# Kernel optimization log

Hardware: AMD Instinct MI355X
Metric: run time of the kernel (lower is better)

Reference implementation:

```python
import jax, jax.numpy as jnp
from jax import lax
import numpy as np

B, N, K = 8, 4096, 64          # clouds, points per cloud, max neighbors
N1, N2 = N // 2, N // 8        # fps ratio 0.5, then 0.25
R1, R2 = 0.2, 0.4              # ball-query radii


def setup_inputs() -> dict:
    key = jax.random.key(0)
    ks = jax.random.split(key, 7)
    def w(k, i, o):
        return jax.random.normal(k, (i, o), jnp.float32) / np.sqrt(i).astype(np.float32)
    return {
        "pos": jax.random.uniform(ks[0], (B, N, 3), jnp.float32),
        "w1a": w(ks[1], 3, 64),    "b1a": jnp.zeros(64, jnp.float32),
        "w1b": w(ks[2], 64, 64),   "b1b": jnp.zeros(64, jnp.float32),
        "w2a": w(ks[3], 67, 128),  "b2a": jnp.zeros(128, jnp.float32),
        "w2b": w(ks[4], 128, 128), "b2b": jnp.zeros(128, jnp.float32),
        "w3a": w(ks[5], 131, 256), "b3a": jnp.zeros(256, jnp.float32),
        "w3b": w(ks[6], 256, 1024),"b3b": jnp.zeros(1024, jnp.float32),
    }


def fps(pos, n_samples):
    # farthest point sampling, deterministic start at index 0. pos: [n, 3]
    d0 = jnp.sum((pos - pos[0]) ** 2, axis=-1)
    def step(mind, _):
        nxt = jnp.argmax(mind)
        d = jnp.sum((pos - pos[nxt]) ** 2, axis=-1)
        return jnp.minimum(mind, d), nxt
    _, idxs = lax.scan(step, d0, None, length=n_samples - 1)
    return jnp.concatenate([jnp.zeros((1,), idxs.dtype), idxs])


def ball_query(centers, pts, r):
    # up to K neighbors within radius r (nearest-first); centers are a subset of pts
    d2 = jnp.sum((centers[:, None, :] - pts[None, :, :]) ** 2, axis=-1)  # [M, n]
    neg = jnp.where(d2 <= r * r, -d2, -jnp.inf)
    vals, nbr = lax.top_k(neg, K)
    return nbr, vals > -jnp.inf  # [M, K] indices, validity mask


def mlp(x, w1, b1, w2, b2, relu_last):
    h = jax.nn.relu(x @ w1 + b1) @ w2 + b2
    return jax.nn.relu(h) if relu_last else h


def masked_max(h, mask):
    # max over neighbor axis; every center has itself as a valid neighbor
    return jnp.max(jnp.where(mask[..., None], h, -jnp.inf), axis=1)


def reference(pos, w1a, b1a, w1b, b1b, w2a, b2a, w2b, b2b, w3a, b3a, w3b, b3b):
    def single(p):  # p: [N, 3]
        # SA1: x is None -> per-edge input is relative position only
        idx1 = fps(p, N1)
        c1 = p[idx1]                                   # [N1, 3]
        nbr1, m1 = ball_query(c1, p, R1)               # [N1, K]
        rel1 = p[nbr1] - c1[:, None, :]                # [N1, K, 3]
        x1 = masked_max(mlp(rel1, w1a, b1a, w1b, b1b, True), m1)   # [N1, 64]
        # SA2: per-edge input is [x_j, pos_j - pos_i]
        idx2 = fps(c1, N2)
        c2 = c1[idx2]                                  # [N2, 3]
        nbr2, m2 = ball_query(c2, c1, R2)              # [N2, K]
        feat2 = jnp.concatenate([x1[nbr2], c1[nbr2] - c2[:, None, :]], axis=-1)  # [N2,K,67]
        x2 = masked_max(mlp(feat2, w2a, b2a, w2b, b2b, True), m2)  # [N2, 128]
        # Global SA: MLP on [x, pos] then global max pool
        g = mlp(jnp.concatenate([x2, c2], axis=-1), w3a, b3a, w3b, b3b, False)   # [N2,1024]
        return jnp.max(g, axis=0)                      # [1024]
    return jax.vmap(single)(pos)                       # [B, 1024]
```

## Files before the change

### kernel.cpp

```cpp
#include <hip/hip_runtime.h>
#include <cstdint>
#include <cstddef>


static constexpr int Bc = 8;
static constexpr int Np = 4096;
static constexpr int Kn = 64;
static constexpr int M1 = 2048;
static constexpr int M2 = 512;
static constexpr int LDX = 132;

#define DEVINL __device__ __forceinline__

DEVINL float d2_exact(float ax, float ay, float az, float bx, float by, float bz) {
    float dx = __fsub_rn(ax, bx);
    float dy = __fsub_rn(ay, by);
    float dz = __fsub_rn(az, bz);
    float xx = __fmul_rn(dx, dx);
    float yy = __fmul_rn(dy, dy);
    float zz = __fmul_rn(dz, dz);
    return __fadd_rn(__fadd_rn(xx, yy), zz);
}

template <int CTRL, int RM, int BM>
DEVINL unsigned long long dpp_max_step(unsigned long long k) {
    unsigned lo = (unsigned)k, hi = (unsigned)(k >> 32);
    unsigned slo = (unsigned)__builtin_amdgcn_update_dpp(0, (int)lo, CTRL, RM, BM, true);
    unsigned shi = (unsigned)__builtin_amdgcn_update_dpp(0, (int)hi, CTRL, RM, BM, true);
    unsigned long long s = ((unsigned long long)shi << 32) | (unsigned long long)slo;
    return s > k ? s : k;
}

DEVINL unsigned long long wave_max_u64_dpp(unsigned long long k) {
    k = dpp_max_step<0x111, 0xf, 0xf>(k);
    k = dpp_max_step<0x112, 0xf, 0xf>(k);
    k = dpp_max_step<0x114, 0xf, 0xf>(k);
    k = dpp_max_step<0x118, 0xf, 0xf>(k);
    k = dpp_max_step<0x142, 0xa, 0xf>(k);
    k = dpp_max_step<0x143, 0xc, 0xf>(k);
    return k;
}

DEVINL unsigned mort3(unsigned v) {
    return (v & 1u) | ((v & 2u) << 2) | ((v & 4u) << 4);
}

DEVINL unsigned cell_of(float x, float y, float z) {
    int ix = (int)(x * 8.0f); ix = ix < 0 ? 0 : (ix > 7 ? 7 : ix);
    int iy = (int)(y * 8.0f); iy = iy < 0 ? 0 : (iy > 7 ? 7 : iy);
    int iz = (int)(z * 8.0f); iz = iz < 0 ? 0 : (iz > 7 ? 7 : iz);
    return mort3((unsigned)ix) | (mort3((unsigned)iy) << 1) | (mort3((unsigned)iz) << 2);
}

DEVINL unsigned* scan512(unsigned* h0, unsigned* h1, int t) {
    unsigned* src = h0; unsigned* dst = h1;
    for (int d = 1; d < 512; d <<= 1) {
        unsigned v = src[t];
        if (t >= d) v += src[t - d];
        dst[t] = v;
        __syncthreads();
        unsigned* tmp = src; src = dst; dst = tmp;
    }
    return src;
}

__global__ __launch_bounds__(512)
void fps2x_kernel(const float* __restrict__ pos, float* __restrict__ c1,
                  float* __restrict__ c2, float* __restrict__ X) {
    constexpr int NT = 512;
    __shared__ float scx[Np], scy[Np], scz[Np];
    __shared__ unsigned spk[Np];
    __shared__ float s2c[M1 * 3];
    __shared__ unsigned h0[512], h1[512];
    __shared__ unsigned long long slots[3];
    const int b = blockIdx.x;
    const int t = threadIdx.x;
    const int lane = t & 63;

    {
        constexpr int PT = Np / NT;
        const float* base = pos + (size_t)b * Np * 3;
        float gx[PT], gy[PT], gz[PT];
        unsigned gc[PT];
        #pragma unroll
        for (int j = 0; j < PT; ++j) {
            int p = j * NT + t;
            gx[j] = base[p * 3 + 0];
            gy[j] = base[p * 3 + 1];
            gz[j] = base[p * 3 + 2];
            gc[j] = cell_of(gx[j], gy[j], gz[j]);
        }
        float x0 = base[0], y0 = base[1], z0 = base[2];
        h0[t] = 0;
        if (t == 0) { slots[0] = 0; slots[1] = 0; slots[2] = 0; }
        __syncthreads();
        #pragma unroll
        for (int j = 0; j < PT; ++j) atomicAdd(&h0[gc[j]], 1u);
        __syncthreads();
        unsigned cnt = h0[t];
        unsigned* inc = scan512(h0, h1, t);
        inc[t] -= cnt;
        __syncthreads();
        #pragma unroll
        for (int j = 0; j < PT; ++j) {
            unsigned p = atomicAdd(&inc[gc[j]], 1u);
            scx[p] = gx[j]; scy[p] = gy[j]; scz[p] = gz[j];
            spk[p] = ((0xFFFu - (unsigned)(j * NT + t)) << 12) | p;
        }
        __syncthreads();

        float px[PT], py[PT], pz[PT], mind[PT];
        unsigned oi[PT];
        #pragma unroll
        for (int j = 0; j < PT; ++j) {
            int p = t * PT + j;
            px[j] = scx[p]; py[j] = scy[p]; pz[j] = scz[p];
            oi[j] = spk[p];
        }
        float lox = px[0], hix = px[0], loy = py[0], hiy = py[0], loz = pz[0], hiz = pz[0];
        #pragma unroll
        for (int j = 1; j < PT; ++j) {
            lox = fminf(lox, px[j]); hix = fmaxf(hix, px[j]);
            loy = fminf(loy, py[j]); hiy = fmaxf(hiy, py[j]);
            loz = fminf(loz, pz[j]); hiz = fmaxf(hiz, pz[j]);
        }

        unsigned long long ck = 0;
        #pragma unroll
        for (int j = 0; j < PT; ++j) {
            float d = d2_exact(px[j], py[j], pz[j], x0, y0, z0);
            mind[j] = d;
            unsigned long long kj =
                ((unsigned long long)__float_as_uint(d) << 24) | (unsigned long long)oi[j];
            if (kj > ck) ck = kj;
        }
        float bmax = __uint_as_float((unsigned)(ck >> 24));
        unsigned long long wkey = wave_max_u64_dpp(ck);
        if (lane == 63) atomicMax(&slots[1], wkey);
        if (t == 0) {
            s2c[0] = x0; s2c[1] = y0; s2c[2] = z0;
        }
        int rd = 1, wr = 2, rs = 0;
        for (int s = 1; s < M1; ++s) {
            __syncthreads();
            unsigned long long km = slots[rd];
            if (t == 0) slots[rs] = 0;
            unsigned spos = (unsigned)km & 0xFFFu;
            float cx = scx[spos], cy = scy[spos], cz = scz[spos];
            if (t == 0) {
                s2c[s * 3 + 0] = cx; s2c[s * 3 + 1] = cy; s2c[s * 3 + 2] = cz;
            }
            float dxv = fmaxf(fmaxf(lox - cx, cx - hix), 0.0f);
            float dyv = fmaxf(fmaxf(loy - cy, cy - hiy), 0.0f);
            float dzv = fmaxf(fmaxf(loz - cz, cz - hiz), 0.0f);
            float L = dxv * dxv + dyv * dyv + dzv * dzv;
            bool fire = (L * 0.999f <= bmax);
            if (fire) {
                unsigned long long nck = 0;
                #pragma unroll
                for (int j = 0; j < PT; ++j) {
                    float d = d2_exact(px[j], py[j], pz[j], cx, cy, cz);
                    float m = fminf(mind[j], d);
                    mind[j] = m;
                    unsigned long long kj =
                        ((unsigned long long)__float_as_uint(m) << 24) | (unsigned long long)oi[j];
                    if (kj > nck) nck = kj;
                }
                ck = nck;
                bmax = __uint_as_float((unsigned)(ck >> 24));
            }
            if (__ballot(fire) != 0ull) wkey = wave_max_u64_dpp(ck);
            if (lane == 63) atomicMax(&slots[wr], wkey);
            int nrd = wr; wr = rs; rs = rd; rd = nrd;
        }
    }
    __syncthreads();

    for (int i = t; i < M1 * 3; i += 512)
        c1[(size_t)b * M1 * 3 + i] = s2c[i];

    {
        constexpr int PT = M1 / NT;
        float* c2buf = s2c;
        float gx[PT], gy[PT], gz[PT];
        unsigned gc[PT];
        #pragma unroll
        for (int j = 0; j < PT; ++j) {
            int p = j * NT + t;
            gx[j] = s2c[p * 3 + 0];
            gy[j] = s2c[p * 3 + 1];
            gz[j] = s2c[p * 3 + 2];
            gc[j] = cell_of(gx[j], gy[j], gz[j]);
        }
        float x0 = s2c[0], y0 = s2c[1], z0 = s2c[2];
        h0[t] = 0;
        if (t == 0) { slots[0] = 0; slots[1] = 0; slots[2] = 0; }
        __syncthreads();
        #pragma unroll
        for (int j = 0; j < PT; ++j) atomicAdd(&h0[gc[j]], 1u);
        __syncthreads();
        unsigned cnt = h0[t];
        unsigned* inc = scan512(h0, h1, t);
        inc[t] -= cnt;
        __syncthreads();
        #pragma unroll
        for (int j = 0; j < PT; ++j) {
            unsigned p = atomicAdd(&inc[gc[j]], 1u);
            scx[p] = gx[j]; scy[p] = gy[j]; scz[p] = gz[j];
            spk[p] = ((0xFFFu - (unsigned)(j * NT + t)) << 12) | p;
        }
        __syncthreads();

        float px[PT], py[PT], pz[PT], mind[PT];
        unsigned oi[PT];
        #pragma unroll
        for (int j = 0; j < PT; ++j) {
            int p = t * PT + j;
            px[j] = scx[p]; py[j] = scy[p]; pz[j] = scz[p];
            oi[j] = spk[p];
        }
        float lox = px[0], hix = px[0], loy = py[0], hiy = py[0], loz = pz[0], hiz = pz[0];
        #pragma unroll
        for (int j = 1; j < PT; ++j) {
            lox = fminf(lox, px[j]); hix = fmaxf(hix, px[j]);
            loy = fminf(loy, py[j]); hiy = fmaxf(hiy, py[j]);
            loz = fminf(loz, pz[j]); hiz = fmaxf(hiz, pz[j]);
        }

        unsigned long long ck = 0;
        #pragma unroll
        for (int j = 0; j < PT; ++j) {
            float d = d2_exact(px[j], py[j], pz[j], x0, y0, z0);
            mind[j] = d;
            unsigned long long kj =
                ((unsigned long long)__float_as_uint(d) << 24) | (unsigned long long)oi[j];
            if (kj > ck) ck = kj;
        }
        float bmax = __uint_as_float((unsigned)(ck >> 24));
        unsigned long long wkey = wave_max_u64_dpp(ck);
        if (lane == 63) atomicMax(&slots[1], wkey);
        if (t == 0) {
            c2buf[0] = x0; c2buf[1] = y0; c2buf[2] = z0;
        }
        int rd = 1, wr = 2, rs = 0;
        for (int s = 1; s < M2; ++s) {
            __syncthreads();
            unsigned long long km = slots[rd];
            if (t == 0) slots[rs] = 0;
            unsigned spos = (unsigned)km & 0xFFFu;
            float cx = scx[spos], cy = scy[spos], cz = scz[spos];
            if (t == 0) {
                c2buf[s * 3 + 0] = cx; c2buf[s * 3 + 1] = cy; c2buf[s * 3 + 2] = cz;
            }
            float dxv = fmaxf(fmaxf(lox - cx, cx - hix), 0.0f);
            float dyv = fmaxf(fmaxf(loy - cy, cy - hiy), 0.0f);
            float dzv = fmaxf(fmaxf(loz - cz, cz - hiz), 0.0f);
            float L = dxv * dxv + dyv * dyv + dzv * dzv;
            bool fire = (L * 0.999f <= bmax);
            if (fire) {
                unsigned long long nck = 0;
                #pragma unroll
                for (int j = 0; j < PT; ++j) {
                    float d = d2_exact(px[j], py[j], pz[j], cx, cy, cz);
                    float m = fminf(mind[j], d);
                    mind[j] = m;
                    unsigned long long kj =
                        ((unsigned long long)__float_as_uint(m) << 24) | (unsigned long long)oi[j];
                    if (kj > nck) nck = kj;
                }
                ck = nck;
                bmax = __uint_as_float((unsigned)(ck >> 24));
            }
            if (__ballot(fire) != 0ull) wkey = wave_max_u64_dpp(ck);
            if (lane == 63) atomicMax(&slots[wr], wkey);
            int nrd = wr; wr = rs; rs = rd; rd = nrd;
        }
        __syncthreads();

        for (int i = t; i < M2 * 3; i += 512)
            c2[(size_t)b * M2 * 3 + i] = c2buf[i];
        for (int i = t; i < M2 * 3; i += 512) {
            int s = i / 3, k = i - s * 3;
            X[(size_t)(b * M2 + s) * LDX + 128 + k] = c2buf[i];
        }
    }
}

template <int NPT>
__global__ __launch_bounds__(256)
void bq_kernel(const float* __restrict__ pts, const float* __restrict__ ctr,
               int mshift, float r2, int* __restrict__ nbr) {
    constexpr int CH = NPT / 64;
    constexpr int CAP = 1024;
    __shared__ uint2 cbuf[4][CAP];
    const int lane = threadIdx.x & 63;
    const int wl = threadIdx.x >> 6;
    int w = __builtin_amdgcn_readfirstlane((int)(blockIdx.x * 4 + wl));
    const int b = w >> mshift;
    const float* pb = pts + (size_t)b * NPT * 3;
    const float* cp = ctr + (size_t)w * 3;
    float cx = cp[0], cy = cp[1], cz = cp[2];
    const unsigned r2b = __float_as_uint(r2);

    unsigned ub[CH];
    int cnt = 0;
    #pragma unroll
    for (int j = 0; j < CH; ++j) {
        int p = j * 64 + lane;
        float d = d2_exact(pb[p * 3 + 0], pb[p * 3 + 1], pb[p * 3 + 2], cx, cy, cz);
        ub[j] = __float_as_uint(d);
        cnt += __popcll(__ballot(ub[j] <= r2b));
    }
    int* out = nbr + (size_t)w * Kn;
    const unsigned long long lml = (1ull << lane) - 1ull;

    if (cnt <= Kn) {
        int basep = 0;
        #pragma unroll
        for (int j = 0; j < CH; ++j) {
            bool v = ub[j] <= r2b;
            unsigned long long mk = __ballot(v);
            if (v) out[basep + __popcll(mk & lml)] = j * 64 + lane;
            basep += __popcll(mk);
        }
        if (lane >= cnt) out[lane] = -1;
    } else if (cnt <= CAP) {
        uint2* buf = cbuf[wl];
        int basep = 0;
        #pragma unroll
        for (int j = 0; j < CH; ++j) {
            bool v = ub[j] <= r2b;
            unsigned long long mk = __ballot(v);
            if (v) buf[basep + __popcll(mk & lml)] =
                       make_uint2(ub[j], (unsigned)(j * 64 + lane));
            basep += __popcll(mk);
        }
        const int C2 = (cnt + 63) >> 6;
        unsigned cb[CAP / 64], ci[CAP / 64];
        #pragma unroll
        for (int e = 0; e < CAP / 64; ++e) {
            if (e >= C2) break;
            int p = e * 64 + lane;
            uint2 v = buf[p];
            cb[e] = (p < cnt) ? v.x : 0xFFFFFFFFu;
            ci[e] = v.y;
        }
        unsigned lo = 0, hi = r2b;
        while (lo < hi) {
            unsigned mid = lo + ((hi - lo) >> 1);
            int c = 0;
            #pragma unroll
            for (int e = 0; e < CAP / 64; ++e) {
                if (e >= C2) break;
                c += __popcll(__ballot(cb[e] <= mid));
            }
            if (c >= Kn) hi = mid; else lo = mid + 1;
        }
        const unsigned tt = lo;
        int cntLess = 0;
        #pragma unroll
        for (int e = 0; e < CAP / 64; ++e) {
            if (e >= C2) break;
            cntLess += __popcll(__ballot(cb[e] < tt));
        }
        const int quota = Kn - cntLess;
        int baseLt = 0, eqseen = 0;
        #pragma unroll
        for (int e = 0; e < CAP / 64; ++e) {
            if (e >= C2) break;
            bool lt = cb[e] < tt;
            bool eq = cb[e] == tt;
            unsigned long long mlt = __ballot(lt);
            unsigned long long meq = __ballot(eq);
            if (lt) out[baseLt + __popcll(mlt & lml)] = (int)ci[e];
            if (eq) {
                int rr = eqseen + __popcll(meq & lml);
                if (rr < quota) out[cntLess + rr] = (int)ci[e];
            }
            baseLt += __popcll(mlt);
            eqseen += __popcll(meq);
        }
    } else {
        unsigned lo = 0, hi = r2b;
        while (lo < hi) {
            unsigned mid = lo + ((hi - lo) >> 1);
            int c = 0;
            #pragma unroll
            for (int j = 0; j < CH; ++j) c += __popcll(__ballot(ub[j] <= mid));
            if (c >= Kn) hi = mid; else lo = mid + 1;
        }
        const unsigned tt = lo;
        int cntLess = 0;
        #pragma unroll
        for (int j = 0; j < CH; ++j) cntLess += __popcll(__ballot(ub[j] < tt));
        const int quota = Kn - cntLess;
        int baseLt = 0, eqseen = 0;
        #pragma unroll
        for (int j = 0; j < CH; ++j) {
            bool lt = ub[j] < tt;
            bool eq = ub[j] == tt;
            unsigned long long mlt = __ballot(lt);
            unsigned long long meq = __ballot(eq);
            if (lt) out[baseLt + __popcll(mlt & lml)] = j * 64 + lane;
            if (eq) {
                int rr = eqseen + __popcll(meq & lml);
                if (rr < quota) out[cntLess + rr] = j * 64 + lane;
            }
            baseLt += __popcll(mlt);
            eqseen += __popcll(meq);
        }
    }
}

__global__ __launch_bounds__(256)
void mlp1_kernel(const float* __restrict__ pos, const float* __restrict__ c1,
                 const int* __restrict__ nbr, const float* __restrict__ w1aT,
                 const float* __restrict__ w1bT, const float* __restrict__ b1b,
                 float* __restrict__ x1) {
    const int lane = threadIdx.x & 63;
    int w = __builtin_amdgcn_readfirstlane((int)(blockIdx.x * 4 + (threadIdx.x >> 6)));
    const int b = w >> 11;
    const int ii = nbr[(size_t)w * Kn + lane];
    const bool valid = ii >= 0;
    const int i2 = valid ? ii : 0;
    const float* pp = pos + ((size_t)b * Np + i2) * 3;
    const float* cc = c1 + (size_t)w * 3;
    float rx = pp[0] - cc[0], ry = pp[1] - cc[1], rz = pp[2] - cc[2];
    float h1[64];
    #pragma unroll
    for (int h = 0; h < 64; ++h) {
        float4 wv = ((const float4*)w1aT)[h];
        float a = fmaf(rx, wv.x, fmaf(ry, wv.y, fmaf(rz, wv.z, wv.w)));
        h1[h] = fmaxf(a, 0.0f);
    }
    float* orow = x1 + (size_t)w * 64;
    for (int c4 = 0; c4 < 16; ++c4) {
        float v4[4];
        #pragma unroll
        for (int cq = 0; cq < 4; ++cq) {
            int c = c4 * 4 + cq;
            float acc = b1b[c];
            const float4* wr = (const float4*)(w1bT + (size_t)c * 64);
            #pragma unroll
            for (int q = 0; q < 16; ++q) {
                float4 wv = wr[q];
                acc = fmaf(h1[4 * q + 0], wv.x, acc);
                acc = fmaf(h1[4 * q + 1], wv.y, acc);
                acc = fmaf(h1[4 * q + 2], wv.z, acc);
                acc = fmaf(h1[4 * q + 3], wv.w, acc);
            }
            float v = fmaxf(acc, 0.0f);
            v = valid ? v : -__builtin_inff();
            #pragma unroll
            for (int o = 32; o > 0; o >>= 1) v = fmaxf(v, __shfl_xor(v, o, 64));
            v4[cq] = v;
        }
        if (lane == 0)
            ((float4*)orow)[c4] = make_float4(v4[0], v4[1], v4[2], v4[3]);
    }
}

__global__ __launch_bounds__(256)
void mlp2_kernel(const float* __restrict__ x1, const float* __restrict__ c1,
                 const float* __restrict__ c2, const int* __restrict__ nbr2,
                 const float* __restrict__ w2aT, const float* __restrict__ w2bT,
                 const float* __restrict__ b2b, float* __restrict__ X) {
    const int lane = threadIdx.x & 63;
    int w = __builtin_amdgcn_readfirstlane((int)(blockIdx.x * 4 + (threadIdx.x >> 6)));
    const int b = w >> 9;
    const int ii = nbr2[(size_t)w * Kn + lane];
    const bool valid = ii >= 0;
    const int i2 = valid ? ii : 0;

    float x[68];
    const float4* xr = (const float4*)(x1 + ((size_t)b * M1 + i2) * 64);
    #pragma unroll
    for (int q = 0; q < 16; ++q) {
        float4 v = xr[q];
        x[4 * q + 0] = v.x; x[4 * q + 1] = v.y;
        x[4 * q + 2] = v.z; x[4 * q + 3] = v.w;
    }
    const float* cc = c2 + (size_t)w * 3;
    const float* cp = c1 + ((size_t)b * M1 + i2) * 3;
    x[64] = cp[0] - cc[0];
    x[65] = cp[1] - cc[1];
    x[66] = cp[2] - cc[2];
    x[67] = 0.0f;

    float h1[128];
    #pragma unroll
    for (int h = 0; h < 128; ++h) {
        const float4* r4 = (const float4*)(w2aT + (size_t)h * 80);
        float acc = 0.0f;
        #pragma unroll
        for (int q = 0; q < 16; ++q) {
            float4 wv = r4[q];
            acc = fmaf(x[4 * q + 0], wv.x, acc);
            acc = fmaf(x[4 * q + 1], wv.y, acc);
            acc = fmaf(x[4 * q + 2], wv.z, acc);
            acc = fmaf(x[4 * q + 3], wv.w, acc);
        }
        float4 tl = r4[16];
        acc = fmaf(x[64], tl.x, acc);
        acc = fmaf(x[65], tl.y, acc);
        acc = fmaf(x[66], tl.z, acc);
        acc += tl.w;
        h1[h] = fmaxf(acc, 0.0f);
    }
    float* orow = X + (size_t)w * LDX;
    for (int c4 = 0; c4 < 32; ++c4) {
        float v4[4];
        #pragma unroll
        for (int cq = 0; cq < 4; ++cq) {
            int c = c4 * 4 + cq;
            float acc = b2b[c];
            const float4* wr = (const float4*)(w2bT + (size_t)c * 128);
            #pragma unroll
            for (int q = 0; q < 32; ++q) {
                float4 wv = wr[q];
                acc = fmaf(h1[4 * q + 0], wv.x, acc);
                acc = fmaf(h1[4 * q + 1], wv.y, acc);
                acc = fmaf(h1[4 * q + 2], wv.z, acc);
                acc = fmaf(h1[4 * q + 3], wv.w, acc);
            }
            float v = fmaxf(acc, 0.0f);
            v = valid ? v : -__builtin_inff();
            #pragma unroll
            for (int o = 32; o > 0; o >>= 1) v = fmaxf(v, __shfl_xor(v, o, 64));
            v4[cq] = v;
        }
        if (lane == 0) {
            orow[c4 * 4 + 0] = v4[0]; orow[c4 * 4 + 1] = v4[1];
            orow[c4 * 4 + 2] = v4[2]; orow[c4 * 4 + 3] = v4[3];
        }
    }
}

__global__ __launch_bounds__(256)
void gemm1_kernel(const float* __restrict__ X, const float* __restrict__ w3a,
                  const float* __restrict__ b3a, float* __restrict__ H) {
    const int r = blockIdx.x;
    const int c = threadIdx.x;
    const float* xr = X + (size_t)r * LDX;
    float acc = b3a[c];
    for (int i = 0; i < 131; ++i)
        acc = fmaf(xr[i], w3a[(size_t)i * 256 + c], acc);
    H[(size_t)r * 256 + c] = fmaxf(acc, 0.0f);
}

__global__ __launch_bounds__(256)
void gemm2_kernel(const float* __restrict__ H, const float* __restrict__ w3b,
                  float* __restrict__ part) {
    __shared__ float As[32][33];
    __shared__ float Bs[32][64];
    __shared__ float red[8][64];
    const int bidx = blockIdx.x;
    const int nt = bidx & 15;
    const int mt = (bidx >> 4) & 15;
    const int b = bidx >> 8;
    const int row0 = b * M2 + mt * 32;
    const int col0 = nt * 64;
    const int t = threadIdx.x;
    const int rg = t >> 5, cg = t & 31;

    float acc[4][2] = {{0.f, 0.f}, {0.f, 0.f}, {0.f, 0.f}, {0.f, 0.f}};
    for (int k0 = 0; k0 < 256; k0 += 32) {
        #pragma unroll
        for (int q = 0; q < 4; ++q) {
            int id = t + q * 256;
            As[id >> 5][id & 31] = H[(size_t)(row0 + (id >> 5)) * 256 + k0 + (id & 31)];
        }
        #pragma unroll
        for (int q = 0; q < 8; ++q) {
            int id = t + q * 256;
            Bs[id >> 6][id & 63] = w3b[(size_t)(k0 + (id >> 6)) * 1024 + col0 + (id & 63)];
        }
        __syncthreads();
        #pragma unroll
        for (int kk = 0; kk < 32; ++kk) {
            float b0 = Bs[kk][cg * 2 + 0];
            float b1 = Bs[kk][cg * 2 + 1];
            #pragma unroll
            for (int j = 0; j < 4; ++j) {
                float a = As[rg * 4 + j][kk];
                acc[j][0] = fmaf(a, b0, acc[j][0]);
                acc[j][1] = fmaf(a, b1, acc[j][1]);
            }
        }
        __syncthreads();
    }
    float m0 = fmaxf(fmaxf(acc[0][0], acc[1][0]), fmaxf(acc[2][0], acc[3][0]));
    float m1 = fmaxf(fmaxf(acc[0][1], acc[1][1]), fmaxf(acc[2][1], acc[3][1]));
    red[rg][cg * 2 + 0] = m0;
    red[rg][cg * 2 + 1] = m1;
    __syncthreads();
    if (t < 64) {
        float v = red[0][t];
        #pragma unroll
        for (int q = 1; q < 8; ++q) v = fmaxf(v, red[q][t]);
        part[((size_t)b * 16 + mt) * 1024 + col0 + t] = v;
    }
}

__global__ __launch_bounds__(256)
void rmax_kernel(const float* __restrict__ part, const float* __restrict__ b3b,
                 float* __restrict__ out) {
    int i = blockIdx.x * 256 + threadIdx.x;
    int b = i >> 10, c = i & 1023;
    float v = -__builtin_inff();
    #pragma unroll
    for (int tt = 0; tt < 16; ++tt)
        v = fmaxf(v, part[((size_t)b * 16 + tt) * 1024 + c]);
    out[i] = v + b3b[c];
}

__global__ __launch_bounds__(256)
void prep_kernel(const float* __restrict__ w1a, const float* __restrict__ b1a,
                 const float* __restrict__ w1b, const float* __restrict__ w2a,
                 const float* __restrict__ b2a, const float* __restrict__ w2b,
                 float* __restrict__ w1aT, float* __restrict__ w1bT,
                 float* __restrict__ w2aT, float* __restrict__ w2bT) {
    int i = blockIdx.x * 256 + threadIdx.x;
    if (i < 64 * 4) {
        int h = i >> 2, d = i & 3;
        w1aT[i] = (d < 3) ? w1a[d * 64 + h] : b1a[h];
    }
    if (i < 64 * 64) {
        int c = i >> 6, h = i & 63;
        w1bT[i] = w1b[h * 64 + c];
    }
    if (i < 128 * 80) {
        int h = i / 80, d = i - h * 80;
        w2aT[i] = (d < 67) ? w2a[d * 128 + h] : ((d == 67) ? b2a[h] : 0.0f);
    }
    {
        int c = i >> 7, h = i & 127;
        w2bT[i] = w2b[h * 128 + c];
    }
}

extern "C" void kernel_launch(void* const* d_in, const int* in_sizes, int n_in,
                              void* d_out, int out_size, void* d_ws, size_t ws_size,
                              hipStream_t stream) {
    const float* pos = (const float*)d_in[0];
    const float* w1a = (const float*)d_in[1];
    const float* b1a = (const float*)d_in[2];
    const float* w1b = (const float*)d_in[3];
    const float* b1b = (const float*)d_in[4];
    const float* w2a = (const float*)d_in[5];
    const float* b2a = (const float*)d_in[6];
    const float* w2b = (const float*)d_in[7];
    const float* b2b = (const float*)d_in[8];
    const float* w3a = (const float*)d_in[9];
    const float* b3a = (const float*)d_in[10];
    const float* w3b = (const float*)d_in[11];
    const float* b3b = (const float*)d_in[12];
    float* out = (float*)d_out;

    char* ws = (char*)d_ws;
    size_t off = 0;
    auto alloc = [&](size_t bytes) -> char* {
        char* p = ws + off;
        off += (bytes + 255) & ~(size_t)255;
        return p;
    };
    float* c1   = (float*)alloc(sizeof(float) * Bc * M1 * 3);
    float* c2   = (float*)alloc(sizeof(float) * Bc * M2 * 3);
    int*   nbr1 = (int*)alloc(sizeof(int) * Bc * M1 * Kn);
    int*   nbr2 = (int*)alloc(sizeof(int) * Bc * M2 * Kn);
    float* x1   = (float*)alloc(sizeof(float) * Bc * M1 * 64);
    float* X    = (float*)alloc(sizeof(float) * Bc * M2 * LDX);
    float* H    = (float*)alloc(sizeof(float) * Bc * M2 * 256);
    float* part = (float*)alloc(sizeof(float) * Bc * 16 * 1024);
    float* w1aT = (float*)alloc(sizeof(float) * 64 * 4);
    float* w1bT = (float*)alloc(sizeof(float) * 64 * 64);
    float* w2aT = (float*)alloc(sizeof(float) * 128 * 80);
    float* w2bT = (float*)alloc(sizeof(float) * 128 * 128);

    prep_kernel<<<dim3(64), dim3(256), 0, stream>>>(w1a, b1a, w1b, w2a, b2a, w2b,
                                                    w1aT, w1bT, w2aT, w2bT);
    fps2x_kernel<<<dim3(Bc), dim3(512), 0, stream>>>(pos, c1, c2, X);
    bq_kernel<Np><<<dim3(Bc * M1 / 4), dim3(256), 0, stream>>>(
        pos, c1, 11, (float)(0.2 * 0.2), nbr1);
    mlp1_kernel<<<dim3(Bc * M1 / 4), dim3(256), 0, stream>>>(
        pos, c1, nbr1, w1aT, w1bT, b1b, x1);
    bq_kernel<M1><<<dim3(Bc * M2 / 4), dim3(256), 0, stream>>>(
        c1, c2, 9, (float)(0.4 * 0.4), nbr2);
    mlp2_kernel<<<dim3(Bc * M2 / 4), dim3(256), 0, stream>>>(
        x1, c1, c2, nbr2, w2aT, w2bT, b2b, X);
    gemm1_kernel<<<dim3(Bc * M2), dim3(256), 0, stream>>>(X, w3a, b3a, H);
    gemm2_kernel<<<dim3(Bc * 16 * 16), dim3(256), 0, stream>>>(H, w3b, part);
    rmax_kernel<<<dim3(32), dim3(256), 0, stream>>>(part, b3b, out);
}
```

Before: 2.569 ms.

## Chunk FPS into staged launches overlapping ball-query and MLP work on spare CUs

The serial farthest-point-sampling loop is split into chunks of 512 (or 256) samples across several launches, with the sorted point cache and min-distance state saved to global memory between chunks. Each launch also gives its extra blocks the fused ball-query plus MLP work for centers that earlier chunks already produced, so SA1/SA2 neighbor search and the MLPs overlap with the latency-bound FPS running on only 8 blocks. Ball query and MLP are fused per wave, which removes the nbr1 and nbr2 global round trips, and the point cache is packed as float4. The cost is reloading FPS state at each chunk boundary, extra launches, and a large shared-memory footprint per block.

```diff
diff --git a/kernel.cpp b/kernel.cpp
--- a/kernel.cpp
+++ b/kernel.cpp
@@ -64,33 +64,35 @@
     return src;
 }
 
-__global__ __launch_bounds__(512)
-void fps2x_kernel(const float* __restrict__ pos, float* __restrict__ c1,
-                  float* __restrict__ c2, float* __restrict__ X) {
-    constexpr int NT = 512;
-    __shared__ float scx[Np], scy[Np], scz[Np];
-    __shared__ unsigned spk[Np];
-    __shared__ float s2c[M1 * 3];
-    __shared__ unsigned h0[512], h1[512];
-    __shared__ unsigned long long slots[3];
-    const int b = blockIdx.x;
-    const int t = threadIdx.x;
-    const int lane = t & 63;
-
-    {
-        constexpr int PT = Np / NT;
-        const float* base = pos + (size_t)b * Np * 3;
+template <int NPTS, int PT>
+DEVINL void fps_chunk_body(const float* __restrict__ srcpts,
+                           float4* __restrict__ scp_g,
+                           float* __restrict__ mind_g,
+                           char* smem, int t, int lane,
+                           int s_begin, int s_end) {
+    constexpr int NT = NPTS / PT;
+    float4* scp = (float4*)smem;
+    unsigned* h0 = (unsigned*)(smem + 65536);
+    unsigned* h1 = (unsigned*)(smem + 67584);
+    unsigned long long* slots = (unsigned long long*)(smem + 69632);
+    float* journal = (float*)(smem + 69664);
+
+    float px[PT], py[PT], pz[PT], mind[PT];
+    unsigned oi[PT];
+    unsigned long long ck = 0;
+
+    if (s_begin == 0) {
         float gx[PT], gy[PT], gz[PT];
         unsigned gc[PT];
         #pragma unroll
         for (int j = 0; j < PT; ++j) {
             int p = j * NT + t;
-            gx[j] = base[p * 3 + 0];
-            gy[j] = base[p * 3 + 1];
-            gz[j] = base[p * 3 + 2];
+            gx[j] = srcpts[p * 3 + 0];
+            gy[j] = srcpts[p * 3 + 1];
+            gz[j] = srcpts[p * 3 + 2];
             gc[j] = cell_of(gx[j], gy[j], gz[j]);
         }
-        float x0 = base[0], y0 = base[1], z0 = base[2];
+        float x0 = srcpts[0], y0 = srcpts[1], z0 = srcpts[2];
         h0[t] = 0;
         if (t == 0) { slots[0] = 0; slots[1] = 0; slots[2] = 0; }
         __syncthreads();
@@ -104,28 +106,17 @@
         #pragma unroll
         for (int j = 0; j < PT; ++j) {
             unsigned p = atomicAdd(&inc[gc[j]], 1u);
-            scx[p] = gx[j]; scy[p] = gy[j]; scz[p] = gz[j];
-            spk[p] = ((0xFFFu - (unsigned)(j * NT + t)) << 12) | p;
-        }
-        __syncthreads();
-
-        float px[PT], py[PT], pz[PT], mind[PT];
-        unsigned oi[PT];
+            unsigned key = ((0xFFFu - (unsigned)(j * NT + t)) << 12) | p;
+            scp[p] = make_float4(gx[j], gy[j], gz[j], __uint_as_float(key));
+        }
+        __syncthreads();
+        for (int k = t; k < NPTS; k += NT) scp_g[k] = scp[k];
         #pragma unroll
         for (int j = 0; j < PT; ++j) {
-            int p = t * PT + j;
-            px[j] = scx[p]; py[j] = scy[p]; pz[j] = scz[p];
-            oi[j] = spk[p];
-        }
-        float lox = px[0], hix = px[0], loy = py[0], hiy = py[0], loz = pz[0], hiz = pz[0];
-        #pragma unroll
-        for (int j = 1; j < PT; ++j) {
-            lox = fminf(lox, px[j]); hix = fmaxf(hix, px[j]);
-            loy = fminf(loy, py[j]); hiy = fmaxf(hiy, py[j]);
-            loz = fminf(loz, pz[j]); hiz = fmaxf(hiz, pz[j]);
-        }
-
-        unsigned long long ck = 0;
+            float4 v = scp[t * PT + j];
+            px[j] = v.x; py[j] = v.y; pz[j] = v.z;
+            oi[j] = __float_as_uint(v.w);
+        }
         #pragma unroll
         for (int j = 0; j < PT; ++j) {
             float d = d2_exact(px[j], py[j], pz[j], x0, y0, z0);
@@ -134,172 +125,85 @@
                 ((unsigned long long)__float_as_uint(d) << 24) | (unsigned long long)oi[j];
             if (kj > ck) ck = kj;
         }
-        float bmax = __uint_as_float((unsigned)(ck >> 24));
-        unsigned long long wkey = wave_max_u64_dpp(ck);
-        if (lane == 63) atomicMax(&slots[1], wkey);
+        if (t == 0) { journal[0] = x0; journal[1] = y0; journal[2] = z0; }
+    } else {
+        if (t == 0) { slots[0] = 0; slots[1] = 0; slots[2] = 0; }
+        for (int k = t; k < NPTS; k += NT) scp[k] = scp_g[k];
+        __syncthreads();
+        #pragma unroll
+        for (int j = 0; j < PT; ++j) {
+            float4 v = scp[t * PT + j];
+            px[j] = v.x; py[j] = v.y; pz[j] = v.z;
+            oi[j] = __float_as_uint(v.w);
+        }
+        #pragma unroll
+        for (int j = 0; j < PT; ++j) mind[j] = mind_g[t * PT + j];
+        #pragma unroll
+        for (int j = 0; j < PT; ++j) {
+            unsigned long long kj =
+                ((unsigned long long)__float_as_uint(mind[j]) << 24) |
+                (unsigned long long)oi[j];
+            if (kj > ck) ck = kj;
+        }
+    }
+
+    float lox = px[0], hix = px[0], loy = py[0], hiy = py[0], loz = pz[0], hiz = pz[0];
+    #pragma unroll
+    for (int j = 1; j < PT; ++j) {
+        lox = fminf(lox, px[j]); hix = fmaxf(hix, px[j]);
+        loy = fminf(loy, py[j]); hiy = fmaxf(hiy, py[j]);
+        loz = fminf(loz, pz[j]); hiz = fmaxf(hiz, pz[j]);
+    }
+
+    float bmax = __uint_as_float((unsigned)(ck >> 24));
+    unsigned long long wkey = wave_max_u64_dpp(ck);
+    if (lane == 63) atomicMax(&slots[1], wkey);
+
+    int rd = 1, wr = 2, rs = 0;
+    for (int s = (s_begin == 0 ? 1 : s_begin); s < s_end; ++s) {
+        __syncthreads();
+        unsigned long long km = slots[rd];
+        if (t == 0) slots[rs] = 0;
+        unsigned spos = (unsigned)km & 0xFFFu;
+        float4 cc = scp[spos];
+        float cx = cc.x, cy = cc.y, cz = cc.z;
         if (t == 0) {
-            s2c[0] = x0; s2c[1] = y0; s2c[2] = z0;
-        }
-        int rd = 1, wr = 2, rs = 0;
-        for (int s = 1; s < M1; ++s) {
-            __syncthreads();
-            unsigned long long km = slots[rd];
-            if (t == 0) slots[rs] = 0;
-            unsigned spos = (unsigned)km & 0xFFFu;
-            float cx = scx[spos], cy = scy[spos], cz = scz[spos];
-            if (t == 0) {
-                s2c[s * 3 + 0] = cx; s2c[s * 3 + 1] = cy; s2c[s * 3 + 2] = cz;
-            }
-            float dxv = fmaxf(fmaxf(lox - cx, cx - hix), 0.0f);
-            float dyv = fmaxf(fmaxf(loy - cy, cy - hiy), 0.0f);
-            float dzv = fmaxf(fmaxf(loz - cz, cz - hiz), 0.0f);
-            float L = dxv * dxv + dyv * dyv + dzv * dzv;
-            bool fire = (L * 0.999f <= bmax);
-            if (fire) {
-                unsigned long long nck = 0;
-                #pragma unroll
-                for (int j = 0; j < PT; ++j) {
-                    float d = d2_exact(px[j], py[j], pz[j], cx, cy, cz);
-                    float m = fminf(mind[j], d);
-                    mind[j] = m;
-                    unsigned long long kj =
-                        ((unsigned long long)__float_as_uint(m) << 24) | (unsigned long long)oi[j];
-                    if (kj > nck) nck = kj;
-                }
-                ck = nck;
-                bmax = __uint_as_float((unsigned)(ck >> 24));
-            }
-            if (__ballot(fire) != 0ull) wkey = wave_max_u64_dpp(ck);
-            if (lane == 63) atomicMax(&slots[wr], wkey);
-            int nrd = wr; wr = rs; rs = rd; rd = nrd;
-        }
+            int jj = (s - s_begin) * 3;
+            journal[jj + 0] = cx; journal[jj + 1] = cy; journal[jj + 2] = cz;
+        }
+        float dxv = fmaxf(fmaxf(lox - cx, cx - hix), 0.0f);
+        float dyv = fmaxf(fmaxf(loy - cy, cy - hiy), 0.0f);
+        float dzv = fmaxf(fmaxf(loz - cz, cz - hiz), 0.0f);
+        float L = dxv * dxv + dyv * dyv + dzv * dzv;
+        bool fire = (L * 0.999f <= bmax);
+        if (fire) {
+            unsigned long long nck = 0;
+            #pragma unroll
+            for (int j = 0; j < PT; ++j) {
+                float d = d2_exact(px[j], py[j], pz[j], cx, cy, cz);
+                float m = fminf(mind[j], d);
+                mind[j] = m;
+                unsigned long long kj =
+                    ((unsigned long long)__float_as_uint(m) << 24) | (unsigned long long)oi[j];
+                if (kj > nck) nck = kj;
+            }
+            ck = nck;
+            bmax = __uint_as_float((unsigned)(ck >> 24));
+        }
+        if (__ballot(fire) != 0ull) wkey = wave_max_u64_dpp(ck);
+        if (lane == 63) atomicMax(&slots[wr], wkey);
+        int nrd = wr; wr = rs; rs = rd; rd = nrd;
     }
     __syncthreads();
-
-    for (int i = t; i < M1 * 3; i += 512)
-        c1[(size_t)b * M1 * 3 + i] = s2c[i];
-
-    {
-        constexpr int PT = M1 / NT;
-        float* c2buf = s2c;
-        float gx[PT], gy[PT], gz[PT];
-        unsigned gc[PT];
-        #pragma unroll
-        for (int j = 0; j < PT; ++j) {
-            int p = j * NT + t;
-            gx[j] = s2c[p * 3 + 0];
-            gy[j] = s2c[p * 3 + 1];
-            gz[j] = s2c[p * 3 + 2];
-            gc[j] = cell_of(gx[j], gy[j], gz[j]);
-        }
-        float x0 = s2c[0], y0 = s2c[1], z0 = s2c[2];
-        h0[t] = 0;
-        if (t == 0) { slots[0] = 0; slots[1] = 0; slots[2] = 0; }
-        __syncthreads();
-        #pragma unroll
-        for (int j = 0; j < PT; ++j) atomicAdd(&h0[gc[j]], 1u);
-        __syncthreads();
-        unsigned cnt = h0[t];
-        unsigned* inc = scan512(h0, h1, t);
-        inc[t] -= cnt;
-        __syncthreads();
-        #pragma unroll
-        for (int j = 0; j < PT; ++j) {
-            unsigned p = atomicAdd(&inc[gc[j]], 1u);
-            scx[p] = gx[j]; scy[p] = gy[j]; scz[p] = gz[j];
-            spk[p] = ((0xFFFu - (unsigned)(j * NT + t)) << 12) | p;
-        }
-        __syncthreads();
-
-        float px[PT], py[PT], pz[PT], mind[PT];
-        unsigned oi[PT];
-        #pragma unroll
-        for (int j = 0; j < PT; ++j) {
-            int p = t * PT + j;
-            px[j] = scx[p]; py[j] = scy[p]; pz[j] = scz[p];
-            oi[j] = spk[p];
-        }
-        float lox = px[0], hix = px[0], loy = py[0], hiy = py[0], loz = pz[0], hiz = pz[0];
-        #pragma unroll
-        for (int j = 1; j < PT; ++j) {
-            lox = fminf(lox, px[j]); hix = fmaxf(hix, px[j]);
-            loy = fminf(loy, py[j]); hiy = fmaxf(hiy, py[j]);
-            loz = fminf(loz, pz[j]); hiz = fmaxf(hiz, pz[j]);
-        }
-
-        unsigned long long ck = 0;
-        #pragma unroll
-        for (int j = 0; j < PT; ++j) {
-            float d = d2_exact(px[j], py[j], pz[j], x0, y0, z0);
-            mind[j] = d;
-            unsigned long long kj =
-                ((unsigned long long)__float_as_uint(d) << 24) | (unsigned long long)oi[j];
-            if (kj > ck) ck = kj;
-        }
-        float bmax = __uint_as_float((unsigned)(ck >> 24));
-        unsigned long long wkey = wave_max_u64_dpp(ck);
-        if (lane == 63) atomicMax(&slots[1], wkey);
-        if (t == 0) {
-            c2buf[0] = x0; c2buf[1] = y0; c2buf[2] = z0;
-        }
-        int rd = 1, wr = 2, rs = 0;
-        for (int s = 1; s < M2; ++s) {
-            __syncthreads();
-            unsigned long long km = slots[rd];
-            if (t == 0) slots[rs] = 0;
-            unsigned spos = (unsigned)km & 0xFFFu;
-            float cx = scx[spos], cy = scy[spos], cz = scz[spos];
-            if (t == 0) {
-                c2buf[s * 3 + 0] = cx; c2buf[s * 3 + 1] = cy; c2buf[s * 3 + 2] = cz;
-            }
-            float dxv = fmaxf(fmaxf(lox - cx, cx - hix), 0.0f);
-            float dyv = fmaxf(fmaxf(loy - cy, cy - hiy), 0.0f);
-            float dzv = fmaxf(fmaxf(loz - cz, cz - hiz), 0.0f);
-            float L = dxv * dxv + dyv * dyv + dzv * dzv;
-            bool fire = (L * 0.999f <= bmax);
-            if (fire) {
-                unsigned long long nck = 0;
-                #pragma unroll
-                for (int j = 0; j < PT; ++j) {
-                    float d = d2_exact(px[j], py[j], pz[j], cx, cy, cz);
-                    float m = fminf(mind[j], d);
-                    mind[j] = m;
-                    unsigned long long kj =
-                        ((unsigned long long)__float_as_uint(m) << 24) | (unsigned long long)oi[j];
-                    if (kj > nck) nck = kj;
-                }
-                ck = nck;
-                bmax = __uint_as_float((unsigned)(ck >> 24));
-            }
-            if (__ballot(fire) != 0ull) wkey = wave_max_u64_dpp(ck);
-            if (lane == 63) atomicMax(&slots[wr], wkey);
-            int nrd = wr; wr = rs; rs = rd; rd = nrd;
-        }
-        __syncthreads();
-
-        for (int i = t; i < M2 * 3; i += 512)
-            c2[(size_t)b * M2 * 3 + i] = c2buf[i];
-        for (int i = t; i < M2 * 3; i += 512) {
-            int s = i / 3, k = i - s * 3;
-            X[(size_t)(b * M2 + s) * LDX + 128 + k] = c2buf[i];
-        }
-    }
+    #pragma unroll
+    for (int j = 0; j < PT; ++j) mind_g[t * PT + j] = mind[j];
 }
 
 template <int NPT>
-__global__ __launch_bounds__(256)
-void bq_kernel(const float* __restrict__ pts, const float* __restrict__ ctr,
-               int mshift, float r2, int* __restrict__ nbr) {
+DEVINL void bq_core(const float* __restrict__ pb, float cx, float cy, float cz,
+                    float r2, int* out, uint2* buf, int lane) {
     constexpr int CH = NPT / 64;
     constexpr int CAP = 1024;
-    __shared__ uint2 cbuf[4][CAP];
-    const int lane = threadIdx.x & 63;
-    const int wl = threadIdx.x >> 6;
-    int w = __builtin_amdgcn_readfirstlane((int)(blockIdx.x * 4 + wl));
-    const int b = w >> mshift;
-    const float* pb = pts + (size_t)b * NPT * 3;
-    const float* cp = ctr + (size_t)w * 3;
-    float cx = cp[0], cy = cp[1], cz = cp[2];
     const unsigned r2b = __float_as_uint(r2);
 
     unsigned ub[CH];
@@ -311,7 +215,6 @@
         ub[j] = __float_as_uint(d);
         cnt += __popcll(__ballot(ub[j] <= r2b));
     }
-    int* out = nbr + (size_t)w * Kn;
     const unsigned long long lml = (1ull << lane) - 1ull;
 
     if (cnt <= Kn) {
@@ -325,7 +228,6 @@
         }
         if (lane >= cnt) out[lane] = -1;
     } else if (cnt <= CAP) {
-        uint2* buf = cbuf[wl];
         int basep = 0;
         #pragma unroll
         for (int j = 0; j < CH; ++j) {
@@ -412,20 +314,15 @@
     }
 }
 
-__global__ __launch_bounds__(256)
-void mlp1_kernel(const float* __restrict__ pos, const float* __restrict__ c1,
-                 const int* __restrict__ nbr, const float* __restrict__ w1aT,
-                 const float* __restrict__ w1bT, const float* __restrict__ b1b,
-                 float* __restrict__ x1) {
-    const int lane = threadIdx.x & 63;
-    int w = __builtin_amdgcn_readfirstlane((int)(blockIdx.x * 4 + (threadIdx.x >> 6)));
-    const int b = w >> 11;
-    const int ii = nbr[(size_t)w * Kn + lane];
+DEVINL void mlp1_core(const float* __restrict__ pb, float cx, float cy, float cz,
+                      const int* nbrL, const float* __restrict__ w1aT,
+                      const float* __restrict__ w1bT, const float* __restrict__ b1b,
+                      float* __restrict__ orow, int lane) {
+    const int ii = nbrL[lane];
     const bool valid = ii >= 0;
     const int i2 = valid ? ii : 0;
-    const float* pp = pos + ((size_t)b * Np + i2) * 3;
-    const float* cc = c1 + (size_t)w * 3;
-    float rx = pp[0] - cc[0], ry = pp[1] - cc[1], rz = pp[2] - cc[2];
+    const float* pp = pb + (size_t)i2 * 3;
+    float rx = pp[0] - cx, ry = pp[1] - cy, rz = pp[2] - cz;
     float h1[64];
     #pragma unroll
     for (int h = 0; h < 64; ++h) {
@@ -433,7 +330,6 @@
         float a = fmaf(rx, wv.x, fmaf(ry, wv.y, fmaf(rz, wv.z, wv.w)));
         h1[h] = fmaxf(a, 0.0f);
     }
-    float* orow = x1 + (size_t)w * 64;
     for (int c4 = 0; c4 < 16; ++c4) {
         float v4[4];
         #pragma unroll
@@ -460,31 +356,27 @@
     }
 }
 
-__global__ __launch_bounds__(256)
-void mlp2_kernel(const float* __restrict__ x1, const float* __restrict__ c1,
-                 const float* __restrict__ c2, const int* __restrict__ nbr2,
-                 const float* __restrict__ w2aT, const float* __restrict__ w2bT,
-                 const float* __restrict__ b2b, float* __restrict__ X) {
-    const int lane = threadIdx.x & 63;
-    int w = __builtin_amdgcn_readfirstlane((int)(blockIdx.x * 4 + (threadIdx.x >> 6)));
-    const int b = w >> 9;
-    const int ii = nbr2[(size_t)w * Kn + lane];
+DEVINL void mlp2_core(const float* __restrict__ x1b, const float* __restrict__ c1b,
+                      float cx, float cy, float cz, const int* nbrL,
+                      const float* __restrict__ w2aT, const float* __restrict__ w2bT,
+                      const float* __restrict__ b2b, float* __restrict__ orow,
+                      int lane) {
+    const int ii = nbrL[lane];
     const bool valid = ii >= 0;
     const int i2 = valid ? ii : 0;
 
     float x[68];
-    const float4* xr = (const float4*)(x1 + ((size_t)b * M1 + i2) * 64);
+    const float4* xr = (const float4*)(x1b + (size_t)i2 * 64);
     #pragma unroll
     for (int q = 0; q < 16; ++q) {
         float4 v = xr[q];
         x[4 * q + 0] = v.x; x[4 * q + 1] = v.y;
         x[4 * q + 2] = v.z; x[4 * q + 3] = v.w;
     }
-    const float* cc = c2 + (size_t)w * 3;
-    const float* cp = c1 + ((size_t)b * M1 + i2) * 3;
-    x[64] = cp[0] - cc[0];
-    x[65] = cp[1] - cc[1];
-    x[66] = cp[2] - cc[2];
+    const float* cp = c1b + (size_t)i2 * 3;
+    x[64] = cp[0] - cx;
+    x[65] = cp[1] - cy;
+    x[66] = cp[2] - cz;
     x[67] = 0.0f;
 
     float h1[128];
@@ -507,7 +399,6 @@
         acc += tl.w;
         h1[h] = fmaxf(acc, 0.0f);
     }
-    float* orow = X + (size_t)w * LDX;
     for (int c4 = 0; c4 < 32; ++c4) {
         float v4[4];
         #pragma unroll
@@ -533,6 +424,113 @@
             orow[c4 * 4 + 0] = v4[0]; orow[c4 * 4 + 1] = v4[1];
             orow[c4 * 4 + 2] = v4[2]; orow[c4 * 4 + 3] = v4[3];
         }
+    }
+}
+
+__global__ __launch_bounds__(512)
+void stage_kernel(int fps_stage, int s_begin, int s_end,
+                  int w_stage, int w_begin, int wsh,
+                  const float* __restrict__ pos, float* __restrict__ c1,
+                  float* __restrict__ c2, float* __restrict__ X,
+                  float* __restrict__ x1,
+                  float4* __restrict__ scp1_g, float* __restrict__ mind1_g,
+                  float4* __restrict__ scp2_g, float* __restrict__ mind2_g,
+                  const float* __restrict__ w1a, const float* __restrict__ b1a,
+                  const float* __restrict__ w1b, const float* __restrict__ w2a,
+                  const float* __restrict__ b2a, const float* __restrict__ w2b,
+                  float* __restrict__ w1aT, float* __restrict__ w1bT,
+                  float* __restrict__ w2aT, float* __restrict__ w2bT,
+                  const float* __restrict__ b1b, const float* __restrict__ b2b) {
+    __shared__ __align__(16) char smem[94720];
+    const int t = threadIdx.x;
+    const int lane = t & 63;
+    const int wid = t >> 6;
+
+    if (fps_stage > 0 && blockIdx.x < Bc) {
+        const int b = blockIdx.x;
+        float* journal = (float*)(smem + 69664);
+        if (fps_stage == 1) {
+            fps_chunk_body<Np, 8>(pos + (size_t)b * Np * 3, scp1_g + (size_t)b * Np,
+                                  mind1_g + (size_t)b * Np, smem, t, lane,
+                                  s_begin, s_end);
+            int n = (s_end - s_begin) * 3;
+            for (int i = t; i < n; i += 512)
+                c1[(size_t)b * M1 * 3 + s_begin * 3 + i] = journal[i];
+        } else {
+            fps_chunk_body<M1, 4>(c1 + (size_t)b * M1 * 3, scp2_g + (size_t)b * M1,
+                                  mind2_g + (size_t)b * M1, smem, t, lane,
+                                  s_begin, s_end);
+            int n = (s_end - s_begin) * 3;
+            for (int i = t; i < n; i += 512)
+                c2[(size_t)b * M2 * 3 + s_begin * 3 + i] = journal[i];
+            for (int i = t; i < n; i += 512) {
+                int s = i / 3, k = i - s * 3;
+                X[(size_t)(b * M2 + s_begin + s) * LDX + 128 + k] = journal[i];
+            }
+        }
+        return;
+    }
+
+    const int wb = (fps_stage > 0) ? (int)blockIdx.x - Bc : (int)blockIdx.x;
+    const int nw = (fps_stage > 0) ? (int)gridDim.x - Bc : (int)gridDim.x;
+
+    if (w_stage == 1) {
+        int i = wb * 512 + t;
+        if (i < 64 * 4) {
+            int h = i >> 2, d = i & 3;
+            w1aT[i] = (d < 3) ? w1a[d * 64 + h] : b1a[h];
+        }
+        if (i < 64 * 64) {
+            int c = i >> 6, h = i & 63;
+            w1bT[i] = w1b[h * 64 + c];
+        }
+        if (i < 128 * 80) {
+            int h = i / 80, d = i - h * 80;
+            w2aT[i] = (d < 67) ? w2a[d * 128 + h] : ((d == 67) ? b2a[h] : 0.0f);
+        }
+        if (i < 128 * 128) {
+            int c = i >> 7, h = i & 127;
+            w2bT[i] = w2b[h * 128 + c];
+        }
+        return;
+    }
+
+    if (w_stage == 2) {
+        uint2* cbuf = (uint2*)smem + (size_t)wid * 1024;
+        int* nbrL = (int*)(smem + 65536) + wid * 64;
+        const int span_mask = (1 << wsh) - 1;
+        const int ntasks = Bc << wsh;
+        for (int task = wb * 8 + wid; task < ntasks; task += nw * 8) {
+            const int b = task >> wsh;
+            const int s = w_begin + (task & span_mask);
+            const int w = b * M1 + s;
+            const float* cr = c1 + (size_t)w * 3;
+            float cx = cr[0], cy = cr[1], cz = cr[2];
+            const float* pb = pos + (size_t)b * Np * 3;
+            bq_core<Np>(pb, cx, cy, cz, (float)(0.2 * 0.2), nbrL, cbuf, lane);
+            mlp1_core(pb, cx, cy, cz, nbrL, w1aT, w1bT, b1b,
+                      x1 + (size_t)w * 64, lane);
+        }
+        return;
+    }
+
+    if (w_stage == 3) {
+        uint2* cbuf = (uint2*)smem + (size_t)wid * 1024;
+        int* nbrL = (int*)(smem + 65536) + wid * 64;
+        const int span_mask = (1 << wsh) - 1;
+        const int ntasks = Bc << wsh;
+        for (int task = wb * 8 + wid; task < ntasks; task += nw * 8) {
+            const int b = task >> wsh;
+            const int s = w_begin + (task & span_mask);
+            const int w = b * M2 + s;
+            const float* cr = c2 + (size_t)w * 3;
+            float cx = cr[0], cy = cr[1], cz = cr[2];
+            const float* c1b = c1 + (size_t)b * M1 * 3;
+            bq_core<M1>(c1b, cx, cy, cz, (float)(0.4 * 0.4), nbrL, cbuf, lane);
+            mlp2_core(x1 + (size_t)b * M1 * 64, c1b, cx, cy, cz, nbrL,
+                      w2aT, w2bT, b2b, X + (size_t)w * LDX, lane);
+        }
+        return;
     }
 }
 
@@ -612,31 +610,6 @@
     for (int tt = 0; tt < 16; ++tt)
         v = fmaxf(v, part[((size_t)b * 16 + tt) * 1024 + c]);
     out[i] = v + b3b[c];
-}
-
-__global__ __launch_bounds__(256)
-void prep_kernel(const float* __restrict__ w1a, const float* __restrict__ b1a,
-                 const float* __restrict__ w1b, const float* __restrict__ w2a,
-                 const float* __restrict__ b2a, const float* __restrict__ w2b,
-                 float* __restrict__ w1aT, float* __restrict__ w1bT,
-                 float* __restrict__ w2aT, float* __restrict__ w2bT) {
-    int i = blockIdx.x * 256 + threadIdx.x;
-    if (i < 64 * 4) {
-        int h = i >> 2, d = i & 3;
-        w1aT[i] = (d < 3) ? w1a[d * 64 + h] : b1a[h];
-    }
-    if (i < 64 * 64) {
-        int c = i >> 6, h = i & 63;
-        w1bT[i] = w1b[h * 64 + c];
-    }
-    if (i < 128 * 80) {
-        int h = i / 80, d = i - h * 80;
-        w2aT[i] = (d < 67) ? w2a[d * 128 + h] : ((d == 67) ? b2a[h] : 0.0f);
-    }
-    {
-        int c = i >> 7, h = i & 127;
-        w2bT[i] = w2b[h * 128 + c];
-    }
 }
 
 extern "C" void kernel_launch(void* const* d_in, const int* in_sizes, int n_in,
@@ -664,30 +637,36 @@
         off += (bytes + 255) & ~(size_t)255;
         return p;
     };
-    float* c1   = (float*)alloc(sizeof(float) * Bc * M1 * 3);
-    float* c2   = (float*)alloc(sizeof(float) * Bc * M2 * 3);
-    int*   nbr1 = (int*)alloc(sizeof(int) * Bc * M1 * Kn);
-    int*   nbr2 = (int*)alloc(sizeof(int) * Bc * M2 * Kn);
-    float* x1   = (float*)alloc(sizeof(float) * Bc * M1 * 64);
-    float* X    = (float*)alloc(sizeof(float) * Bc * M2 * LDX);
-    float* H    = (float*)alloc(sizeof(float) * Bc * M2 * 256);
-    float* part = (float*)alloc(sizeof(float) * Bc * 16 * 1024);
-    float* w1aT = (float*)alloc(sizeof(float) * 64 * 4);
-    float* w1bT = (float*)alloc(sizeof(float) * 64 * 64);
-    float* w2aT = (float*)alloc(sizeof(float) * 128 * 80);
-    float* w2bT = (float*)alloc(sizeof(float) * 128 * 128);
-
-    prep_kernel<<<dim3(64), dim3(256), 0, stream>>>(w1a, b1a, w1b, w2a, b2a, w2b,
-                                                    w1aT, w1bT, w2aT, w2bT);
-    fps2x_kernel<<<dim3(Bc), dim3(512), 0, stream>>>(pos, c1, c2, X);
-    bq_kernel<Np><<<dim3(Bc * M1 / 4), dim3(256), 0, stream>>>(
-        pos, c1, 11, (float)(0.2 * 0.2), nbr1);
-    mlp1_kernel<<<dim3(Bc * M1 / 4), dim3(256), 0, stream>>>(
-        pos, c1, nbr1, w1aT, w1bT, b1b, x1);
-    bq_kernel<M1><<<dim3(Bc * M2 / 4), dim3(256), 0, stream>>>(
-        c1, c2, 9, (float)(0.4 * 0.4), nbr2);
-    mlp2_kernel<<<dim3(Bc * M2 / 4), dim3(256), 0, stream>>>(
-        x1, c1, c2, nbr2, w2aT, w2bT, b2b, X);
+    float*  c1     = (float*)alloc(sizeof(float) * Bc * M1 * 3);
+    float*  c2     = (float*)alloc(sizeof(float) * Bc * M2 * 3);
+    float*  x1     = (float*)alloc(sizeof(float) * Bc * M1 * 64);
+    float*  X      = (float*)alloc(sizeof(float) * Bc * M2 * LDX);
+    float*  H      = (float*)alloc(sizeof(float) * Bc * M2 * 256);
+    float*  part   = (float*)alloc(sizeof(float) * Bc * 16 * 1024);
+    float*  w1aT   = (float*)alloc(sizeof(float) * 64 * 4);
+    float*  w1bT   = (float*)alloc(sizeof(float) * 64 * 64);
+    float*  w2aT   = (float*)alloc(sizeof(float) * 128 * 80);
+    float*  w2bT   = (float*)alloc(sizeof(float) * 128 * 128);
+    float4* scp1_g = (float4*)alloc(sizeof(float4) * Bc * Np);
+    float*  mind1g = (float*)alloc(sizeof(float) * Bc * Np);
+    float4* scp2_g = (float4*)alloc(sizeof(float4) * Bc * M1);
+    float*  mind2g = (float*)alloc(sizeof(float) * Bc * M1);
+
+    auto launch = [&](int grid, int fs, int sb, int se, int wsg, int wbg, int wsh) {
+        stage_kernel<<<dim3(grid), dim3(512), 0, stream>>>(
+            fs, sb, se, wsg, wbg, wsh,
+            pos, c1, c2, X, x1, scp1_g, mind1g, scp2_g, mind2g,
+            w1a, b1a, w1b, w2a, b2a, w2b, w1aT, w1bT, w2aT, w2bT, b1b, b2b);
+    };
+
+    launch(Bc + 32, 1, 0, 512, 1, 0, 0);
+    launch(Bc + 240, 1, 512, 1024, 2, 0, 9);
+    launch(Bc + 240, 1, 1024, 1536, 2, 512, 9);
+    launch(Bc + 240, 1, 1536, 2048, 2, 1024, 9);
+    launch(Bc + 240, 2, 0, 256, 2, 1536, 9);
+    launch(Bc + 240, 2, 256, 512, 3, 0, 8);
+    launch(240, 0, 0, 0, 3, 256, 8);
+
     gemm1_kernel<<<dim3(Bc * M2), dim3(256), 0, stream>>>(X, w3a, b3a, H);
     gemm2_kernel<<<dim3(Bc * 16 * 16), dim3(256), 0, stream>>>(H, w3b, part);
     rmax_kernel<<<dim3(32), dim3(256), 0, stream>>>(part, b3b, out);
```

Result: slower. 3.407 ms (+32.7%).
